# Kernel tuning notes

Measured on AMD Instinct MI355X. Metric: run time of the kernel, lower is better.

The kernel has to match this reference:

```python
import jax, jax.numpy as jnp
import numpy as np

M, K, D = 8, 4096, 512  # groups, codes per group, total dim
DG = D // M             # per-group dim = 64


def setup_inputs() -> dict:
    key = jax.random.key(0)
    k1, k2, k3 = jax.random.split(key, 3)
    codes = jax.random.randint(k1, (32, 64, 64, M), 0, K, dtype=jnp.int32)
    codebook = jax.random.normal(k2, (M, K, DG), dtype=jnp.float32)
    wv = jax.random.normal(k3, (M, DG, DG), dtype=jnp.float32) / np.sqrt(DG)
    return {"codes": codes, "codebook": codebook, "wv": wv}


def reference(codes, codebook, wv):
    # v[m,k,c] = sum_d codebook[m,k,d] * wv[m,c,d]  (small per-group GEMM)
    v = jnp.einsum('mkd,mcd->mkc', codebook, wv)  # [M, K, DG]
    # one-hot matmul over k is exactly an indexed gather:
    # gathered[n,h,w,m,c] = v[m, codes[n,h,w,m], c]
    m_idx = jnp.arange(v.shape[0])  # [M]
    gathered = v[m_idx[None, None, None, :], codes]  # [n,h,w,M,DG]
    n, h, w = codes.shape[:3]
    out = gathered.reshape(n, h, w, -1)          # [n,h,w,D]
    return jnp.transpose(out, (0, 3, 1, 2))      # [n,D,h,w]
```

## Files before the change

kernel.cpp:

```cpp
#include <hip/hip_runtime.h>

#define MQ 8
#define KQ 4096
#define DG 64
#define NN 32
#define HW 4096
#define DD 512

typedef float f32x4 __attribute__((ext_vector_type(4)));

__global__ __launch_bounds__(256) void compute_v_kernel(
    const float* __restrict__ codebook,
    const float* __restrict__ wv,
    float* __restrict__ v) {
  __shared__ float wv_t[DG][DG + 1];
  __shared__ float cb[64][DG];

  const int m = blockIdx.y;
  const int k0 = blockIdx.x * 64;
  const int tid = threadIdx.x;

  const float4* wvm4 = (const float4*)(wv + (size_t)m * DG * DG);
  for (int i = tid; i < DG * DG / 4; i += 256) {
    int c = i >> 4, d4 = (i & 15) * 4;
    float4 val = wvm4[i];
    wv_t[d4 + 0][c] = val.x;
    wv_t[d4 + 1][c] = val.y;
    wv_t[d4 + 2][c] = val.z;
    wv_t[d4 + 3][c] = val.w;
  }
  const float4* cbm4 = (const float4*)(codebook + ((size_t)m * KQ + k0) * DG);
  float4* cb4 = (float4*)&cb[0][0];
  for (int i = tid; i < 64 * DG / 4; i += 256) cb4[i] = cbm4[i];
  __syncthreads();

  const int c = tid & 63;
  const int kq = tid >> 6;

  float acc[16];
#pragma unroll
  for (int kl = 0; kl < 16; ++kl) acc[kl] = 0.f;

  for (int d4 = 0; d4 < DG; d4 += 4) {
    float w0 = wv_t[d4 + 0][c];
    float w1 = wv_t[d4 + 1][c];
    float w2 = wv_t[d4 + 2][c];
    float w3 = wv_t[d4 + 3][c];
#pragma unroll
    for (int kl = 0; kl < 16; ++kl) {
      float4 cbv = *(const float4*)&cb[kq * 16 + kl][d4];
      acc[kl] += cbv.x * w0 + cbv.y * w1 + cbv.z * w2 + cbv.w * w3;
    }
  }

  float* vout = v + ((size_t)(m * 16 + (c >> 2)) * KQ) * 4 + (c & 3);
#pragma unroll
  for (int kl = 0; kl < 16; ++kl) {
    vout[(size_t)(k0 + kq * 16 + kl) * 4] = acc[kl];
  }
}

__global__ __launch_bounds__(256, 4) void gather_direct_kernel(
    const int* __restrict__ codes,
    const float* __restrict__ v,
    float* __restrict__ out) {
  const int b = blockIdx.x;
  const int m = b & 7;
  const int chunk = (b >> 3) & 3;
  const int n = b >> 5;

  const int tid = threadIdx.x;
  const int hw0 = chunk * 1024 + 4 * tid;

  const int* cp = codes + ((size_t)n * HW + hw0) * MQ + m;
  const int r0 = cp[0 * MQ];
  const int r1 = cp[1 * MQ];
  const int r2 = cp[2 * MQ];
  const int r3 = cp[3 * MQ];

  const f32x4* vq = (const f32x4*)v + (size_t)m * 16 * KQ;
  float* ob = out + ((size_t)n * DD + m * DG) * HW + hw0;

#pragma unroll
  for (int cq = 0; cq < 16; ++cq) {
    const f32x4* plane = vq + (size_t)cq * KQ;
    f32x4 v0 = plane[r0];
    f32x4 v1 = plane[r1];
    f32x4 v2 = plane[r2];
    f32x4 v3 = plane[r3];
    f32x4 o0 = {v0.x, v1.x, v2.x, v3.x};
    f32x4 o1 = {v0.y, v1.y, v2.y, v3.y};
    f32x4 o2 = {v0.z, v1.z, v2.z, v3.z};
    f32x4 o3 = {v0.w, v1.w, v2.w, v3.w};
    float* oc = ob + (size_t)(cq * 4) * HW;
    __builtin_nontemporal_store(o0, (f32x4*)(oc + 0 * HW));
    __builtin_nontemporal_store(o1, (f32x4*)(oc + 1 * HW));
    __builtin_nontemporal_store(o2, (f32x4*)(oc + 2 * HW));
    __builtin_nontemporal_store(o3, (f32x4*)(oc + 3 * HW));
  }
}

extern "C" void kernel_launch(void* const* d_in, const int* in_sizes, int n_in,
                              void* d_out, int out_size, void* d_ws, size_t ws_size,
                              hipStream_t stream) {
  const int* codes = (const int*)d_in[0];
  const float* codebook = (const float*)d_in[1];
  const float* wv = (const float*)d_in[2];
  float* out = (float*)d_out;
  float* v = (float*)d_ws;

  compute_v_kernel<<<dim3(64, 8), 256, 0, stream>>>(codebook, wv, v);
  gather_direct_kernel<<<NN * 4 * MQ, 256, 0, stream>>>(codes, v, out);
}
```

Before: 305.4 us.

## Store v in 32-wide channel planes and gather with 8 lanes per code

The intermediate v table now uses two 32-channel planes per group instead of sixteen 4-channel planes. In the gather kernel, 8 adjacent lanes read one contiguous 128-byte row per code rather than each lane doing scattered 16-byte loads. Each thread now loops over 8 position chunks and 2 planes, and groups of 8 lanes cover 4 consecutive spatial positions each. The aim is better coalescing of the random gather loads. The trade-off is that output stores are now only 16 bytes contiguous per 8-lane group across channels, and codes are reloaded redundantly by each lane in the group.

```diff
diff --git a/kernel.cpp b/kernel.cpp
--- a/kernel.cpp
+++ b/kernel.cpp
@@ -53,14 +53,14 @@
     }
   }
 
-  float* vout = v + ((size_t)(m * 16 + (c >> 2)) * KQ) * 4 + (c & 3);
+  float* vout = v + ((size_t)(m * 2 + (c >> 5)) * KQ) * 32 + (c & 31);
 #pragma unroll
   for (int kl = 0; kl < 16; ++kl) {
-    vout[(size_t)(k0 + kq * 16 + kl) * 4] = acc[kl];
+    vout[(size_t)(k0 + kq * 16 + kl) * 32] = acc[kl];
   }
 }
 
-__global__ __launch_bounds__(256, 4) void gather_direct_kernel(
+__global__ __launch_bounds__(256, 4) void gather_oct_kernel(
     const int* __restrict__ codes,
     const float* __restrict__ v,
     float* __restrict__ out) {
@@ -70,33 +70,38 @@
   const int n = b >> 5;
 
   const int tid = threadIdx.x;
-  const int hw0 = chunk * 1024 + 4 * tid;
+  const int w = tid >> 6;
+  const int l = tid & 63;
+  const int oc8 = l >> 3;
+  const int lo = l & 7;
 
-  const int* cp = codes + ((size_t)n * HW + hw0) * MQ + m;
-  const int r0 = cp[0 * MQ];
-  const int r1 = cp[1 * MQ];
-  const int r2 = cp[2 * MQ];
-  const int r3 = cp[3 * MQ];
+  const float* vm = v + (size_t)m * 2 * KQ * 32;
+  const int* cp = codes + (size_t)n * HW * MQ + m;
+  float* ob = out + ((size_t)n * DD + m * DG) * HW;
 
-  const f32x4* vq = (const f32x4*)v + (size_t)m * 16 * KQ;
-  float* ob = out + ((size_t)n * DD + m * DG) * HW + hw0;
+  for (int p = 0; p < 8; ++p) {
+    const int hwq = chunk * 1024 + p * 128 + w * 32 + oc8 * 4;
+    int r[4];
+#pragma unroll
+    for (int t = 0; t < 4; ++t) r[t] = cp[(size_t)(hwq + t) * MQ];
 
 #pragma unroll
-  for (int cq = 0; cq < 16; ++cq) {
-    const f32x4* plane = vq + (size_t)cq * KQ;
-    f32x4 v0 = plane[r0];
-    f32x4 v1 = plane[r1];
-    f32x4 v2 = plane[r2];
-    f32x4 v3 = plane[r3];
-    f32x4 o0 = {v0.x, v1.x, v2.x, v3.x};
-    f32x4 o1 = {v0.y, v1.y, v2.y, v3.y};
-    f32x4 o2 = {v0.z, v1.z, v2.z, v3.z};
-    f32x4 o3 = {v0.w, v1.w, v2.w, v3.w};
-    float* oc = ob + (size_t)(cq * 4) * HW;
-    __builtin_nontemporal_store(o0, (f32x4*)(oc + 0 * HW));
-    __builtin_nontemporal_store(o1, (f32x4*)(oc + 1 * HW));
-    __builtin_nontemporal_store(o2, (f32x4*)(oc + 2 * HW));
-    __builtin_nontemporal_store(o3, (f32x4*)(oc + 3 * HW));
+    for (int g = 0; g < 2; ++g) {
+      const float* plane = vm + (size_t)g * KQ * 32;
+      f32x4 v0 = *(const f32x4*)(plane + (size_t)r[0] * 32 + lo * 4);
+      f32x4 v1 = *(const f32x4*)(plane + (size_t)r[1] * 32 + lo * 4);
+      f32x4 v2 = *(const f32x4*)(plane + (size_t)r[2] * 32 + lo * 4);
+      f32x4 v3 = *(const f32x4*)(plane + (size_t)r[3] * 32 + lo * 4);
+      f32x4 o0 = {v0.x, v1.x, v2.x, v3.x};
+      f32x4 o1 = {v0.y, v1.y, v2.y, v3.y};
+      f32x4 o2 = {v0.z, v1.z, v2.z, v3.z};
+      f32x4 o3 = {v0.w, v1.w, v2.w, v3.w};
+      float* oc = ob + (size_t)(g * 32 + lo * 4) * HW + hwq;
+      __builtin_nontemporal_store(o0, (f32x4*)(oc + 0 * HW));
+      __builtin_nontemporal_store(o1, (f32x4*)(oc + 1 * HW));
+      __builtin_nontemporal_store(o2, (f32x4*)(oc + 2 * HW));
+      __builtin_nontemporal_store(o3, (f32x4*)(oc + 3 * HW));
+    }
   }
 }
 
@@ -110,5 +115,5 @@
   float* v = (float*)d_ws;
 
   compute_v_kernel<<<dim3(64, 8), 256, 0, stream>>>(codebook, wv, v);
-  gather_direct_kernel<<<NN * 4 * MQ, 256, 0, stream>>>(codes, v, out);
+  gather_oct_kernel<<<NN * 4 * MQ, 256, 0, stream>>>(codes, v, out);
 }
```

Result: no change. 302.3 us (-1.0%).
